# Optimization experiments

Measured on AMD Instinct MI355X. Metric: run time of the kernel, lower is better.

## Reference

```python
import jax, jax.numpy as jnp
import numpy as np

B = 8192; L = 50; D_EMB = 128
N_USER = 100000; N_MOVIE = 50000; N_DENSE = 8
D = 2 * D_EMB + D_EMB + N_DENSE  # 392 total_input_dim
E = 4; T = 2; H1 = 256; H2 = 128; ATT_H = 64; N_CROSS = 3


def setup_inputs() -> dict:
    key = jax.random.key(0)
    ks = jax.random.split(key, 28)
    rn = lambda k, shape, s=0.02: jax.random.normal(k, shape, jnp.float32) * s
    inp = {
        'userId': jax.random.randint(ks[0], (B,), 0, N_USER),
        'movieId': jax.random.randint(ks[1], (B,), 0, N_MOVIE),
        'seq_history': jax.random.randint(ks[2], (B, L), 0, N_MOVIE),
        'dense_feats': jax.random.normal(ks[3], (B, N_DENSE), jnp.float32),
        # embeddings (row 0 is padding_idx -> zeros)
        'emb_user': rn(ks[4], (N_USER + 1, D_EMB)).at[0].set(0.0),
        'emb_movie': rn(ks[5], (N_MOVIE + 1, D_EMB)).at[0].set(0.0),
        # DIN attention MLP: input [q,k,q-k,q*k] = 4*D_EMB
        'att_w1': rn(ks[6], (4 * D_EMB, ATT_H)), 'att_b1': jnp.zeros((ATT_H,), jnp.float32),
        'att_w2': rn(ks[7], (ATT_H, 1)), 'att_b2': jnp.zeros((1,), jnp.float32),
        # LayerNorms
        'in_gamma': jnp.ones((D,), jnp.float32), 'in_beta': jnp.zeros((D,), jnp.float32),
        'cr_gamma': jnp.ones((D,), jnp.float32), 'cr_beta': jnp.zeros((D,), jnp.float32),
        # CrossNetV2: x_{l+1} = x0 * (x_l W_l + b_l) + x_l
        'cross_W': rn(ks[8], (N_CROSS, D, D)), 'cross_b': jnp.zeros((N_CROSS, D), jnp.float32),
        # MMoE experts: Linear(D,H1)-ReLU-Linear(H1,H2), batched over E
        'exp_w1': rn(ks[9], (E, D, H1)), 'exp_b1': jnp.zeros((E, H1), jnp.float32),
        'exp_w2': rn(ks[10], (E, H1, H2)), 'exp_b2': jnp.zeros((E, H2), jnp.float32),
        # gates per task
        'gate_w': rn(ks[11], (T, D, E)), 'gate_b': jnp.zeros((T, E), jnp.float32),
        # task heads Linear(H2, 1)
        'head_w': rn(ks[12], (T, H2)), 'head_b': jnp.zeros((T,), jnp.float32),
    }
    return inp


def _layernorm(x, g, b, eps=1e-5):
    m = jnp.mean(x, axis=-1, keepdims=True)
    v = jnp.var(x, axis=-1, keepdims=True)
    return (x - m) * jax.lax.rsqrt(v + eps) * g + b


def _forward(userId, movieId, seq_history, dense_feats, emb_user, emb_movie,
             att_w1, att_b1, att_w2, att_b2, in_gamma, in_beta,
             cross_W, cross_b, cr_gamma, cr_beta,
             exp_w1, exp_b1, exp_w2, exp_b2, gate_w, gate_b, head_w, head_b):
    # sparse embedding gathers
    user_e = emb_user[userId]            # [B, D_EMB]
    movie_e = emb_movie[movieId]         # [B, D_EMB]  (target item)
    hist = emb_movie[seq_history]        # [B, L, D_EMB]
    mask = seq_history > 0               # [B, L]

    # DIN attention pooling
    q = jnp.broadcast_to(movie_e[:, None, :], hist.shape)            # [B, L, D_EMB]
    att_in = jnp.concatenate([q, hist, q - hist, q * hist], axis=-1)  # [B, L, 4*D_EMB]
    scores = (jax.nn.relu(att_in @ att_w1 + att_b1) @ att_w2 + att_b2)[..., 0]  # [B, L]
    scores = jnp.where(mask, scores, -1e9)
    probs = jax.nn.softmax(scores, axis=-1)                           # [B, L]
    interest = jnp.einsum('bl,bld->bd', probs, hist)                  # [B, D_EMB]

    x = jnp.concatenate([user_e, movie_e, interest, dense_feats], axis=-1)  # [B, D]
    x = _layernorm(x, in_gamma, in_beta)

    # CrossNetV2
    x0 = x
    for l in range(N_CROSS):
        x = x0 * (x @ cross_W[l] + cross_b[l]) + x
    x = _layernorm(x, cr_gamma, cr_beta)

    # MMoE: batched expert GEMMs + per-task soft gates
    h = jax.nn.relu(jnp.einsum('bd,edh->ebh', x, exp_w1) + exp_b1[:, None, :])  # [E,B,H1]
    eo = jnp.einsum('ebh,eho->ebo', h, exp_w2) + exp_b2[:, None, :]             # [E,B,H2]
    g = jax.nn.softmax(jnp.einsum('bd,tde->tbe', x, gate_w) + gate_b[:, None, :], axis=-1)  # [T,B,E]
    task_feat = jnp.einsum('tbe,ebo->tbo', g, eo)                                # [T,B,H2]

    logits = jnp.einsum('tbo,to->tb', task_feat, head_w) + head_b[:, None]       # [T,B]
    return logits


def reference(userId, movieId, seq_history, dense_feats, emb_user, emb_movie,
              att_w1, att_b1, att_w2, att_b2, in_gamma, in_beta,
              cross_W, cross_b, cr_gamma, cr_beta,
              exp_w1, exp_b1, exp_w2, exp_b2, gate_w, gate_b, head_w, head_b):
    return _forward(userId, movieId, seq_history, dense_feats, emb_user, emb_movie,
                    att_w1, att_b1, att_w2, att_b2, in_gamma, in_beta,
                    cross_W, cross_b, cr_gamma, cr_beta,
                    exp_w1, exp_b1, exp_w2, exp_b2, gate_w, gate_b, head_w, head_b)
```

## Files before the change

kernel.cpp:

```cpp
#include <hip/hip_runtime.h>
#include <hip/hip_bf16.h>

typedef short short8 __attribute__((ext_vector_type(8)));
typedef short short4v __attribute__((ext_vector_type(4)));
typedef float f32x4 __attribute__((ext_vector_type(4)));

constexpr int BB = 8192;
constexpr int LL = 50;
constexpr int DE = 128;
constexpr int DD = 392;
constexpr int HH1 = 256;
constexpr int HH2 = 128;

__device__ __forceinline__ short f2b(float x) {
    __hip_bfloat16 h = __float2bfloat16(x);
    return __builtin_bit_cast(short, h);
}
__device__ __forceinline__ float b2f(short v) {
    unsigned u = ((unsigned)(unsigned short)v) << 16;
    return __builtin_bit_cast(float, u);
}

constexpr int S0 = 3 * 392 * 392;
constexpr int S1 = 4 * 392 * 256;
constexpr int S2 = (50001 * 128) / 4;
constexpr int NB_TRANS = 9619;
constexpr int QC0 = 36 + NB_TRANS;
constexpr int NB_PREP = QC0 + 2048;

__global__ __launch_bounds__(256) void prep_all(
    const float* __restrict__ w1,
    const float* __restrict__ w2, const float* __restrict__ b2,
    const float* __restrict__ head_w, const float* __restrict__ att_b1,
    const float* __restrict__ cross_W, const float* __restrict__ exp_w1,
    const float* __restrict__ emb_movie, const int* __restrict__ movieId,
    float* __restrict__ WkpFf, float* __restrict__ hw2, float* __restrict__ hc,
    short* __restrict__ WTc, short* __restrict__ WT1, short* __restrict__ embB,
    float* __restrict__ qcAll)
{
    __shared__ float sh[4][128];
    const int blk = blockIdx.x, t = threadIdx.x;

    if (blk < 32) {
        int o = blk * 256 + t;
        int e = o & 7, lane = (o >> 3) & 63, nt = (o >> 9) & 3, kt = o >> 11;
        int k = (kt << 5) + ((lane >> 4) << 3) + e;
        int h = (nt << 4) + (lane & 15);
        int base = (o >> 3) << 4;
        WkpFf[base + e]     = w1[(128 + k) * 64 + h] - w1[(256 + k) * 64 + h];
        WkpFf[base + 8 + e] = w1[(384 + k) * 64 + h];
    } else if (blk < 36) {
        const int e = blk - 32;
        float* hw = &sh[0][0];
        hw[t] = head_w[t];
        __syncthreads();
        const float* row = &w2[((long)e * HH1 + t) * HH2];
        float s0 = 0.f, s1 = 0.f;
        #pragma unroll 8
        for (int o = 0; o < 128; o += 4) {
            float4 v = *reinterpret_cast<const float4*>(&row[o]);
            s0 += v.x * hw[o] + v.y * hw[o + 1] + v.z * hw[o + 2] + v.w * hw[o + 3];
            s1 += v.x * hw[128 + o] + v.y * hw[129 + o] + v.z * hw[130 + o] + v.w * hw[131 + o];
        }
        hw2[(((e << 8) + t) << 1) + 0] = s0;
        hw2[(((e << 8) + t) << 1) + 1] = s1;
        if (t < 2) {
            float s = 0.f;
            for (int o = 0; o < 128; ++o) s += b2[e * 128 + o] * hw[t * 128 + o];
            hc[e * 2 + t] = s;
        }
    } else if (blk < QC0) {
        int idx = (blk - 36) * 256 + t;
        if (idx < S0) {
            int z = idx / (392 * 392), rr = idx - z * 392 * 392;
            int c = rr / 392, r = rr - c * 392;
            WTc[idx] = f2b(cross_W[(long)z * 153664 + r * 392 + c]);
        } else if (idx < S0 + S1) {
            int j = idx - S0;
            int z = j / 100352, rr = j - z * 100352;
            int c = rr / 392, r = rr - c * 392;
            WT1[j] = f2b(exp_w1[(long)z * 100352 + r * 256 + c]);
        } else if (idx < S0 + S1 + S2) {
            long j = (long)(idx - S0 - S1) << 2;
            float4 v = *reinterpret_cast<const float4*>(&emb_movie[j]);
            short4v o;
            o[0] = f2b(v.x); o[1] = f2b(v.y); o[2] = f2b(v.z); o[3] = f2b(v.w);
            *reinterpret_cast<short4v*>(&embB[j]) = o;
        }
    } else {
        const int w = t >> 6, lane = t & 63;
        const int b = (blk - QC0) * 4 + w;
        if (lane < 32)
            *reinterpret_cast<float4*>(&sh[w][lane << 2]) =
                *reinterpret_cast<const float4*>(
                    &emb_movie[(long)movieId[b] * DE + (lane << 2)]);
        __syncthreads();
        float s = att_b1[lane];
        #pragma unroll 8
        for (int d = 0; d < 128; ++d)
            s = fmaf(sh[w][d], w1[d * 64 + lane] + w1[16384 + d * 64 + lane], s);
        qcAll[((long)b << 6) + lane] = s;
    }
}

__global__ __launch_bounds__(256, 8) void attn_kernel(
    const int* __restrict__ userId, const int* __restrict__ movieId,
    const int* __restrict__ seq, const float* __restrict__ dense,
    const float* __restrict__ emb_user, const float* __restrict__ emb_movie,
    const short* __restrict__ embB,
    const float* __restrict__ qcAll, const float* __restrict__ WkpFf,
    const float* __restrict__ att_w2, const float* __restrict__ att_b2,
    const float* __restrict__ in_gamma, const float* __restrict__ in_beta,
    float* __restrict__ x0f, short* __restrict__ x0b)
{
    __shared__ short hist[64 * 128];
    __shared__ float qs[128];
    __shared__ int   seq_s[64];
    __shared__ float spS[4][64];
    __shared__ float probs[64];
    __shared__ float ibuf[4][128];
    __shared__ float stats[2];

    const int b = blockIdx.x;
    const int t = threadIdx.x;
    const int lane = t & 63;
    const int w = t >> 6;

    if (t < 128) qs[t] = emb_movie[(long)movieId[b] * DE + t];
    if (t < 64)  seq_s[t] = (t < LL) ? seq[b * LL + t] : 0;
    __syncthreads();

    #pragma unroll
    for (int i = 0; i < 4; ++i) {
        const int idx = t + (i << 8);
        const int l = idx >> 4, c = idx & 15;
        short8 hv = *reinterpret_cast<const short8*>(&embB[(long)seq_s[l] * DE + (c << 3)]);
        const int byte = (l << 8) + ((c << 4) ^ ((l & 7) << 4));
        *reinterpret_cast<short8*>(reinterpret_cast<char*>(hist) + byte) = hv;
    }

    const int col = (w << 4) + (lane & 15);
    float ue = (t < 128) ? emb_user[(long)userId[b] * DE + t] : 0.f;
    float dv = (t >= 128 && t < 136) ? dense[b * 8 + (t - 128)] : 0.f;
    const float qc  = qcAll[((long)b << 6) + col];
    const float w2v = att_w2[col];

    short8 bfrag[4];
    #pragma unroll
    for (int kt = 0; kt < 4; ++kt) {
        const float* wkp = &WkpFf[((((kt << 2) + w) << 6) | lane) << 4];
        const int kq = (kt << 5) + ((lane >> 4) << 3);
        #pragma unroll
        for (int j = 0; j < 8; ++j)
            bfrag[kt][j] = f2b(fmaf(qs[kq + j], wkp[8 + j], wkp[j]));
    }
    __syncthreads();

    #pragma unroll
    for (int mt = 0; mt < 4; ++mt) {
        f32x4 acc = {0.f, 0.f, 0.f, 0.f};
        const int row = (mt << 4) + (lane & 15);
        const int rbase = row << 8;
        const int swz = (row & 7) << 4;
        #pragma unroll
        for (int kt = 0; kt < 4; ++kt) {
            const int kbyte = (kt << 6) + ((lane >> 4) << 4);
            short8 a = *reinterpret_cast<const short8*>(
                reinterpret_cast<char*>(hist) + rbase + (kbyte ^ swz));
            acc = __builtin_amdgcn_mfma_f32_16x16x32_bf16(a, bfrag[kt], acc, 0, 0, 0);
        }
        #pragma unroll
        for (int r = 0; r < 4; ++r) {
            float v = fmaxf(acc[r] + qc, 0.f) * w2v;
            v += __shfl_xor(v, 1); v += __shfl_xor(v, 2);
            v += __shfl_xor(v, 4); v += __shfl_xor(v, 8);
            if ((lane & 15) == 0)
                spS[w][(mt << 4) + ((lane >> 4) << 2) + r] = v;
        }
    }
    __syncthreads();

    if (t < 64) {
        float sc = spS[0][t] + spS[1][t] + spS[2][t] + spS[3][t] + att_b2[0];
        float s = (t < LL) ? ((seq_s[t] > 0) ? sc : -1e9f) : -INFINITY;
        float m = s;
        #pragma unroll
        for (int off = 32; off > 0; off >>= 1) m = fmaxf(m, __shfl_xor(m, off));
        float e = (t < LL) ? __expf(s - m) : 0.f;
        float sum = e;
        #pragma unroll
        for (int off = 32; off > 0; off >>= 1) sum += __shfl_xor(sum, off);
        probs[t] = (t < LL) ? (e / sum) : 0.f;
    }
    __syncthreads();

    const int g  = t >> 5;
    const int d0 = (t & 31) << 2;
    float4 ps = make_float4(0.f, 0.f, 0.f, 0.f);
    #pragma unroll
    for (int i = 0; i < 8; ++i) {
        const int l = g + (i << 3);
        const int byte = (l << 8) + ((d0 << 1) ^ ((l & 7) << 4));
        short4v hv = *reinterpret_cast<const short4v*>(
            reinterpret_cast<const char*>(hist) + byte);
        const float p = probs[l];
        ps.x = fmaf(p, b2f(hv[0]), ps.x);
        ps.y = fmaf(p, b2f(hv[1]), ps.y);
        ps.z = fmaf(p, b2f(hv[2]), ps.z);
        ps.w = fmaf(p, b2f(hv[3]), ps.w);
    }
    ps.x += __shfl_xor(ps.x, 32); ps.y += __shfl_xor(ps.y, 32);
    ps.z += __shfl_xor(ps.z, 32); ps.w += __shfl_xor(ps.w, 32);
    if (lane < 32)
        *reinterpret_cast<float4*>(&ibuf[w][(lane & 31) << 2]) = ps;
    __syncthreads();

    float v0 = (t < 128) ? ue : qs[t - 128];
    float v1 = 0.f;
    if (t < 128)       v1 = ibuf[0][t] + ibuf[1][t] + ibuf[2][t] + ibuf[3][t];
    else if (t < 136)  v1 = dv;

    float s2 = v0 + v1, q2 = v0 * v0 + v1 * v1;
    #pragma unroll
    for (int off = 32; off > 0; off >>= 1) {
        s2 += __shfl_xor(s2, off);
        q2 += __shfl_xor(q2, off);
    }
    if (lane == 0) { spS[0][w] = s2; spS[1][w] = q2; }
    __syncthreads();
    if (t == 0) {
        float S = spS[0][0] + spS[0][1] + spS[0][2] + spS[0][3];
        float Q = spS[1][0] + spS[1][1] + spS[1][2] + spS[1][3];
        float mean = S / (float)DD;
        float var = Q / (float)DD - mean * mean;
        stats[0] = mean;
        stats[1] = rsqrtf(var + 1e-5f);
    }
    __syncthreads();
    const float mean = stats[0], inv = stats[1];
    const long base = (long)b * DD;
    float o0 = (v0 - mean) * inv * in_gamma[t] + in_beta[t];
    x0f[base + t] = o0; x0b[base + t] = f2b(o0);
    if (t < 136) {
        float o1 = (v1 - mean) * inv * in_gamma[256 + t] + in_beta[256 + t];
        x0f[base + 256 + t] = o1; x0b[base + 256 + t] = f2b(o1);
    }
}

template<int MODE, int WF32, int WB16, int NXB, int NZB>
__global__ __launch_bounds__(256) void bgemm(
    const short* __restrict__ A, const short* __restrict__ WT,
    const float* __restrict__ bias,
    float* __restrict__ outF, short* __restrict__ outB,
    const float* __restrict__ x0, const float* __restrict__ xin,
    int M, int N, int K, long aZ, long wZ, long bZ, long oZ)
{
    __shared__ short As[2][64 * 64];
    __shared__ short Bs[2][64 * 64];

    int id = blockIdx.x;
    const int qq = (int)gridDim.x >> 3;
    id = (id & 7) * qq + (id >> 3);
    const int mb  = id / (NXB * NZB);
    const int rem = id - mb * (NXB * NZB);
    const int z   = rem / NXB;
    const int xb  = rem - z * NXB;

    A += (long)z * aZ; WT += (long)z * wZ; bias += (long)z * bZ;
    const long oz = (long)z * oZ;

    const int t = threadIdx.x, w = t >> 6, lane = t & 63;
    const int m0 = mb * 64, n0 = xb * 64;
    const int sm = t >> 3, sk8 = (t & 7) << 3;

    f32x4 acc[4];
    #pragma unroll
    for (int i = 0; i < 4; ++i) {
        #pragma unroll
        for (int r = 0; r < 4; ++r) acc[i][r] = 0.f;
    }

    const int nsteps = (K + 63) >> 6;
    short8 avA[2], bvA[2];

    auto loadA = [&](int k0) {
        #pragma unroll
        for (int i = 0; i < 2; ++i) {
            const int r = sm + (i << 5);
            short8 zv = {0, 0, 0, 0, 0, 0, 0, 0};
            avA[i] = zv; bvA[i] = zv;
            if (k0 + sk8 < K) {
                avA[i] = *reinterpret_cast<const short8*>(&A[(long)(m0 + r) * K + k0 + sk8]);
                if (n0 + r < N)
                    bvA[i] = *reinterpret_cast<const short8*>(&WT[(long)(n0 + r) * K + k0 + sk8]);
            }
        }
    };
    auto wrA = [&](int buf) {
        #pragma unroll
        for (int i = 0; i < 2; ++i) {
            const int r = sm + (i << 5);
            const int byte = (r << 7) + ((sk8 << 1) ^ ((r & 7) << 4));
            *reinterpret_cast<short8*>(reinterpret_cast<char*>(&As[buf][0]) + byte) = avA[i];
            *reinterpret_cast<short8*>(reinterpret_cast<char*>(&Bs[buf][0]) + byte) = bvA[i];
        }
    };
    auto domfma = [&](int buf) {
        #pragma unroll
        for (int kt = 0; kt < 2; ++kt) {
            const int kbyte = (kt << 6) + ((lane >> 4) << 4);
            const int ar = (w << 4) + (lane & 15);
            short8 a = *reinterpret_cast<const short8*>(
                reinterpret_cast<char*>(&As[buf][0]) + (ar << 7) + (kbyte ^ ((ar & 7) << 4)));
            #pragma unroll
            for (int nt = 0; nt < 4; ++nt) {
                const int br = (nt << 4) + (lane & 15);
                short8 bb = *reinterpret_cast<const short8*>(
                    reinterpret_cast<char*>(&Bs[buf][0]) + (br << 7) + (kbyte ^ ((br & 7) << 4)));
                acc[nt] = __builtin_amdgcn_mfma_f32_16x16x32_bf16(a, bb, acc[nt], 0, 0, 0);
            }
        }
    };

    loadA(0);
    wrA(0);
    if (nsteps > 1) loadA(64);
    __syncthreads();

    int cur = 0;
    for (int s = 0; s + 1 < nsteps; ++s) {
        domfma(cur);
        wrA(cur ^ 1);
        if (s + 2 < nsteps) loadA((s + 2) << 6);
        __syncthreads();
        cur ^= 1;
    }
    domfma(cur);

    #pragma unroll
    for (int nt = 0; nt < 4; ++nt) {
        const int col = n0 + (nt << 4) + (lane & 15);
        if (col < N) {
            const float bv = bias[col];
            #pragma unroll
            for (int r = 0; r < 4; ++r) {
                const int row = m0 + (w << 4) + ((lane >> 4) << 2) + r;
                float v = acc[nt][r] + bv;
                if (MODE == 1) v = fmaxf(v, 0.f);
                const long o = (long)row * N + col;
                if (MODE == 2) v = x0[o] * v + xin[o];
                if (WF32) outF[oz + o] = v;
                if (WB16) outB[oz + o] = f2b(v);
            }
        }
    }
}

__global__ __launch_bounds__(256) void ln_kernel(
    const float* __restrict__ in,
    const float* __restrict__ gamma, const float* __restrict__ beta,
    short* __restrict__ outB)
{
    __shared__ float red[2][4];
    __shared__ float stats[2];
    const int b = blockIdx.x, t = threadIdx.x, lane = t & 63, w = t >> 6;
    const long base = (long)b * DD;
    float v0 = in[base + t];
    float v1 = (t < 136) ? in[base + 256 + t] : 0.f;
    float s = v0 + v1, q2 = v0 * v0 + v1 * v1;
    #pragma unroll
    for (int off = 32; off > 0; off >>= 1) {
        s += __shfl_xor(s, off);
        q2 += __shfl_xor(q2, off);
    }
    if (lane == 0) { red[0][w] = s; red[1][w] = q2; }
    __syncthreads();
    if (t == 0) {
        float S = red[0][0] + red[0][1] + red[0][2] + red[0][3];
        float Q = red[1][0] + red[1][1] + red[1][2] + red[1][3];
        float mean = S / (float)DD;
        float var = Q / (float)DD - mean * mean;
        stats[0] = mean;
        stats[1] = rsqrtf(var + 1e-5f);
    }
    __syncthreads();
    const float mean = stats[0], inv = stats[1];
    outB[base + t] = f2b((v0 - mean) * inv * gamma[t] + beta[t]);
    if (t < 136)
        outB[base + 256 + t] = f2b((v1 - mean) * inv * gamma[256 + t] + beta[256 + t]);
}

__global__ __launch_bounds__(256) void final_kernel(
    const short* __restrict__ x, const short* __restrict__ h1,
    const float* __restrict__ hw2, const float* __restrict__ hc,
    const float* __restrict__ gate_w, const float* __restrict__ gate_b,
    const float* __restrict__ head_b, float* __restrict__ out)
{
    const int t = threadIdx.x, lane = t & 63, w = t >> 6;
    const int b = blockIdx.x * 4 + w;
    const short* xr = x + (long)b * DD;

    float xv[7];
    #pragma unroll
    for (int i = 0; i < 7; ++i) {
        int d = lane + (i << 6);
        xv[i] = (d < DD) ? b2f(xr[d]) : 0.f;
    }

    float gl[8] = {0.f, 0.f, 0.f, 0.f, 0.f, 0.f, 0.f, 0.f};
    #pragma unroll
    for (int i = 0; i < 7; ++i) {
        int d = lane + (i << 6);
        if (d < DD) {
            float4 g0 = *reinterpret_cast<const float4*>(&gate_w[d << 2]);
            float4 g1 = *reinterpret_cast<const float4*>(&gate_w[1568 + (d << 2)]);
            gl[0] = fmaf(xv[i], g0.x, gl[0]); gl[1] = fmaf(xv[i], g0.y, gl[1]);
            gl[2] = fmaf(xv[i], g0.z, gl[2]); gl[3] = fmaf(xv[i], g0.w, gl[3]);
            gl[4] = fmaf(xv[i], g1.x, gl[4]); gl[5] = fmaf(xv[i], g1.y, gl[5]);
            gl[6] = fmaf(xv[i], g1.z, gl[6]); gl[7] = fmaf(xv[i], g1.w, gl[7]);
        }
    }

    float ed[8];
    #pragma unroll
    for (int e = 0; e < 4; ++e) {
        short4v hv = *reinterpret_cast<const short4v*>(
            &h1[((long)e * BB + b) * HH1 + (lane << 2)]);
        const float* hwp = &hw2[(((e << 8) + (lane << 2))) << 1];
        float4 w01 = *reinterpret_cast<const float4*>(hwp);
        float4 w23 = *reinterpret_cast<const float4*>(hwp + 4);
        float h0 = b2f(hv[0]), h1f = b2f(hv[1]), h2 = b2f(hv[2]), h3 = b2f(hv[3]);
        ed[e]     = fmaf(h0, w01.x, fmaf(h1f, w01.z, fmaf(h2, w23.x, h3 * w23.z)));
        ed[4 + e] = fmaf(h0, w01.y, fmaf(h1f, w01.w, fmaf(h2, w23.y, h3 * w23.w)));
    }

    #pragma unroll
    for (int v = 0; v < 8; ++v) {
        #pragma unroll
        for (int off = 32; off > 0; off >>= 1) {
            gl[v] += __shfl_xor(gl[v], off);
            ed[v] += __shfl_xor(ed[v], off);
        }
    }

    if (lane == 0) {
        float res[2];
        #pragma unroll
        for (int tt = 0; tt < 2; ++tt) {
            float lv[4], m = -1e30f;
            #pragma unroll
            for (int e = 0; e < 4; ++e) {
                lv[e] = gl[tt * 4 + e] + gate_b[tt * 4 + e];
                m = fmaxf(m, lv[e]);
            }
            float sum = 0.f, acc = 0.f;
            #pragma unroll
            for (int e = 0; e < 4; ++e) { lv[e] = __expf(lv[e] - m); sum += lv[e]; }
            #pragma unroll
            for (int e = 0; e < 4; ++e)
                acc = fmaf(lv[e], ed[tt * 4 + e] + hc[e * 2 + tt], acc);
            res[tt] = head_b[tt] + acc / sum;
        }
        out[b] = res[0];
        out[BB + b] = res[1];
    }
}

extern "C" void kernel_launch(void* const* d_in, const int* in_sizes, int n_in,
                              void* d_out, int out_size, void* d_ws, size_t ws_size,
                              hipStream_t stream) {
    const int*   userId    = (const int*)d_in[0];
    const int*   movieId   = (const int*)d_in[1];
    const int*   seq       = (const int*)d_in[2];
    const float* dense     = (const float*)d_in[3];
    const float* emb_user  = (const float*)d_in[4];
    const float* emb_movie = (const float*)d_in[5];
    const float* att_w1    = (const float*)d_in[6];
    const float* att_b1    = (const float*)d_in[7];
    const float* att_w2    = (const float*)d_in[8];
    const float* att_b2    = (const float*)d_in[9];
    const float* in_gamma  = (const float*)d_in[10];
    const float* in_beta   = (const float*)d_in[11];
    const float* cr_gamma  = (const float*)d_in[12];
    const float* cr_beta   = (const float*)d_in[13];
    const float* cross_W   = (const float*)d_in[14];
    const float* cross_b   = (const float*)d_in[15];
    const float* exp_w1    = (const float*)d_in[16];
    const float* exp_b1    = (const float*)d_in[17];
    const float* exp_w2    = (const float*)d_in[18];
    const float* exp_b2    = (const float*)d_in[19];
    const float* gate_w    = (const float*)d_in[20];
    const float* gate_b    = (const float*)d_in[21];
    const float* head_w    = (const float*)d_in[22];
    const float* head_b    = (const float*)d_in[23];
    float* outp = (float*)d_out;

    char* p = (char*)d_ws;
    auto alloc = [&](size_t bytes) -> char* {
        char* r = p; p += (bytes + 255) & ~(size_t)255; return r;
    };
    float* WkpFf = (float*)alloc(16384 * 4);
    float* hw2 = (float*)alloc(2048 * 4);
    float* hc  = (float*)alloc(8 * 4);
    short* WTc = (short*)alloc((size_t)3 * 392 * 392 * 2);
    short* WT1 = (short*)alloc((size_t)4 * 256 * 392 * 2);
    short* embB = (short*)alloc((size_t)50001 * 128 * 2);
    float* qcAll = (float*)alloc((size_t)BB * 64 * 4);
    float* x0f = (float*)alloc((size_t)BB * DD * 4);
    short* x0b = (short*)alloc((size_t)BB * DD * 2);
    float* xAf = (float*)alloc((size_t)BB * DD * 4);
    short* xAb = (short*)alloc((size_t)BB * DD * 2);
    float* xBf = (float*)alloc((size_t)BB * DD * 4);
    short* xBb = (short*)alloc((size_t)BB * DD * 2);
    float* xCf = (float*)alloc((size_t)BB * DD * 4);
    short* xDb = (short*)alloc((size_t)BB * DD * 2);
    short* h1b = (short*)alloc((size_t)4 * BB * HH1 * 2);

    prep_all<<<NB_PREP, 256, 0, stream>>>(
        att_w1, exp_w2, exp_b2, head_w, att_b1, cross_W, exp_w1,
        emb_movie, movieId, WkpFf, hw2, hc, WTc, WT1, embB, qcAll);

    attn_kernel<<<BB, 256, 0, stream>>>(userId, movieId, seq, dense,
                                        emb_user, emb_movie, embB,
                                        qcAll, WkpFf, att_w2, att_b2,
                                        in_gamma, in_beta, x0f, x0b);

    bgemm<2, 1, 1, 7, 1><<<896, 256, 0, stream>>>(x0b, WTc, cross_b, xAf, xAb,
                                                  x0f, x0f, BB, DD, DD, 0, 0, 0, 0);
    bgemm<2, 1, 1, 7, 1><<<896, 256, 0, stream>>>(xAb, WTc + 392 * 392, cross_b + 392,
                                                  xBf, xBb, x0f, xAf, BB, DD, DD, 0, 0, 0, 0);
    bgemm<2, 1, 0, 7, 1><<<896, 256, 0, stream>>>(xBb, WTc + 2 * 392 * 392, cross_b + 784,
                                                  xCf, nullptr, x0f, xBf, BB, DD, DD, 0, 0, 0, 0);

    ln_kernel<<<BB, 256, 0, stream>>>(xCf, cr_gamma, cr_beta, xDb);

    bgemm<1, 0, 1, 4, 4><<<2048, 256, 0, stream>>>(
        xDb, WT1, exp_b1, nullptr, h1b, nullptr, nullptr,
        BB, HH1, DD, 0, (long)HH1 * DD, HH1, (long)BB * HH1);

    final_kernel<<<BB / 4, 256, 0, stream>>>(xDb, h1b, hw2, hc,
                                             gate_w, gate_b, head_b, outp);

    (void)in_sizes; (void)n_in; (void)out_size; (void)ws_size;
}
```

Measured before the change: 177.3 us.

## Enlarge GEMM block tile to 256x64 with 4x4 MFMA register tiling

The batched GEMM now computes a 256x64 output tile per block, with each wave owning a 64x64 sub-tile held in 16 accumulators, and the K step drops to 32. The LDS layout changes to a k-slice-major arrangement with no swizzle. The aim is more reuse of each B fragment across M tiles and less redundant global traffic per FLOP. The cost is higher register pressure and a quarter as many blocks (224 per cross layer), which may leave many CUs idle on a large-CU GPU, plus possible LDS bank conflicts now that the XOR swizzle is gone.

```diff
diff --git a/kernel.cpp b/kernel.cpp
--- a/kernel.cpp
+++ b/kernel.cpp
@@ -248,15 +248,15 @@
 }
 
 template<int MODE, int WF32, int WB16, int NXB, int NZB>
-__global__ __launch_bounds__(256) void bgemm(
+__global__ __launch_bounds__(256) void bgemm2(
     const short* __restrict__ A, const short* __restrict__ WT,
     const float* __restrict__ bias,
     float* __restrict__ outF, short* __restrict__ outB,
     const float* __restrict__ x0, const float* __restrict__ xin,
     int M, int N, int K, long aZ, long wZ, long bZ, long oZ)
 {
-    __shared__ short As[2][64 * 64];
-    __shared__ short Bs[2][64 * 64];
+    __shared__ short As[2][4][256][8];
+    __shared__ short Bs[2][4][64][8];
 
     int id = blockIdx.x;
     const int qq = (int)gridDim.x >> 3;
@@ -270,68 +270,71 @@
     const long oz = (long)z * oZ;
 
     const int t = threadIdx.x, w = t >> 6, lane = t & 63;
-    const int m0 = mb * 64, n0 = xb * 64;
-    const int sm = t >> 3, sk8 = (t & 7) << 3;
-
-    f32x4 acc[4];
-    #pragma unroll
-    for (int i = 0; i < 4; ++i) {
-        #pragma unroll
-        for (int r = 0; r < 4; ++r) acc[i][r] = 0.f;
-    }
-
-    const int nsteps = (K + 63) >> 6;
-    short8 avA[2], bvA[2];
-
-    auto loadA = [&](int k0) {
-        #pragma unroll
-        for (int i = 0; i < 2; ++i) {
-            const int r = sm + (i << 5);
+    const int m0 = mb * 256, n0 = xb * 64;
+    const int brow = t >> 2, bks = t & 3;
+
+    f32x4 acc[4][4];
+    #pragma unroll
+    for (int i = 0; i < 4; ++i)
+        #pragma unroll
+        for (int j = 0; j < 4; ++j)
+            #pragma unroll
+            for (int r = 0; r < 4; ++r) acc[i][j][r] = 0.f;
+
+    const int nsteps = (K + 31) >> 5;
+    short8 avr[4], bvr;
+
+    auto loadr = [&](int k0) {
+        #pragma unroll
+        for (int i = 0; i < 4; ++i) {
+            const int c = t + (i << 8);
+            const int row = c >> 2, ks = c & 3;
+            const int kk = k0 + (ks << 3);
             short8 zv = {0, 0, 0, 0, 0, 0, 0, 0};
-            avA[i] = zv; bvA[i] = zv;
-            if (k0 + sk8 < K) {
-                avA[i] = *reinterpret_cast<const short8*>(&A[(long)(m0 + r) * K + k0 + sk8]);
-                if (n0 + r < N)
-                    bvA[i] = *reinterpret_cast<const short8*>(&WT[(long)(n0 + r) * K + k0 + sk8]);
-            }
-        }
+            avr[i] = (kk < K)
+                ? *reinterpret_cast<const short8*>(&A[(long)(m0 + row) * K + kk]) : zv;
+        }
+        const int kkb = k0 + (bks << 3);
+        short8 zv = {0, 0, 0, 0, 0, 0, 0, 0};
+        bvr = (kkb < K && n0 + brow < N)
+            ? *reinterpret_cast<const short8*>(&WT[(long)(n0 + brow) * K + kkb]) : zv;
     };
-    auto wrA = [&](int buf) {
-        #pragma unroll
-        for (int i = 0; i < 2; ++i) {
-            const int r = sm + (i << 5);
-            const int byte = (r << 7) + ((sk8 << 1) ^ ((r & 7) << 4));
-            *reinterpret_cast<short8*>(reinterpret_cast<char*>(&As[buf][0]) + byte) = avA[i];
-            *reinterpret_cast<short8*>(reinterpret_cast<char*>(&Bs[buf][0]) + byte) = bvA[i];
-        }
+    auto wr = [&](int buf) {
+        #pragma unroll
+        for (int i = 0; i < 4; ++i) {
+            const int c = t + (i << 8);
+            const int row = c >> 2, ks = c & 3;
+            *reinterpret_cast<short8*>(&As[buf][ks][row][0]) = avr[i];
+        }
+        *reinterpret_cast<short8*>(&Bs[buf][bks][brow][0]) = bvr;
     };
     auto domfma = [&](int buf) {
-        #pragma unroll
-        for (int kt = 0; kt < 2; ++kt) {
-            const int kbyte = (kt << 6) + ((lane >> 4) << 4);
-            const int ar = (w << 4) + (lane & 15);
-            short8 a = *reinterpret_cast<const short8*>(
-                reinterpret_cast<char*>(&As[buf][0]) + (ar << 7) + (kbyte ^ ((ar & 7) << 4)));
+        const int ks = lane >> 4, l15 = lane & 15;
+        short8 bf[4];
+        #pragma unroll
+        for (int nt = 0; nt < 4; ++nt)
+            bf[nt] = *reinterpret_cast<const short8*>(&Bs[buf][ks][(nt << 4) + l15][0]);
+        #pragma unroll
+        for (int mt = 0; mt < 4; ++mt) {
+            short8 af = *reinterpret_cast<const short8*>(
+                &As[buf][ks][(w << 6) + (mt << 4) + l15][0]);
             #pragma unroll
-            for (int nt = 0; nt < 4; ++nt) {
-                const int br = (nt << 4) + (lane & 15);
-                short8 bb = *reinterpret_cast<const short8*>(
-                    reinterpret_cast<char*>(&Bs[buf][0]) + (br << 7) + (kbyte ^ ((br & 7) << 4)));
-                acc[nt] = __builtin_amdgcn_mfma_f32_16x16x32_bf16(a, bb, acc[nt], 0, 0, 0);
-            }
+            for (int nt = 0; nt < 4; ++nt)
+                acc[mt][nt] = __builtin_amdgcn_mfma_f32_16x16x32_bf16(
+                    af, bf[nt], acc[mt][nt], 0, 0, 0);
         }
     };
 
-    loadA(0);
-    wrA(0);
-    if (nsteps > 1) loadA(64);
+    loadr(0);
+    wr(0);
+    if (nsteps > 1) loadr(32);
     __syncthreads();
 
     int cur = 0;
     for (int s = 0; s + 1 < nsteps; ++s) {
         domfma(cur);
-        wrA(cur ^ 1);
-        if (s + 2 < nsteps) loadA((s + 2) << 6);
+        wr(cur ^ 1);
+        if (s + 2 < nsteps) loadr((s + 2) << 5);
         __syncthreads();
         cur ^= 1;
     }
@@ -339,18 +342,21 @@
 
     #pragma unroll
     for (int nt = 0; nt < 4; ++nt) {
-        const int col = n0 + (nt << 4) + (lane & 15);
-        if (col < N) {
-            const float bv = bias[col];
+        const int c = n0 + (nt << 4) + (lane & 15);
+        if (c < N) {
+            const float bv = bias[c];
             #pragma unroll
-            for (int r = 0; r < 4; ++r) {
-                const int row = m0 + (w << 4) + ((lane >> 4) << 2) + r;
-                float v = acc[nt][r] + bv;
-                if (MODE == 1) v = fmaxf(v, 0.f);
-                const long o = (long)row * N + col;
-                if (MODE == 2) v = x0[o] * v + xin[o];
-                if (WF32) outF[oz + o] = v;
-                if (WB16) outB[oz + o] = f2b(v);
+            for (int mt = 0; mt < 4; ++mt) {
+                #pragma unroll
+                for (int r = 0; r < 4; ++r) {
+                    const int row = m0 + (w << 6) + (mt << 4) + ((lane >> 4) << 2) + r;
+                    float v = acc[mt][nt][r] + bv;
+                    if (MODE == 1) v = fmaxf(v, 0.f);
+                    const long o = (long)row * N + c;
+                    if (MODE == 2) v = x0[o] * v + xin[o];
+                    if (WF32) outF[oz + o] = v;
+                    if (WB16) outB[oz + o] = f2b(v);
+                }
             }
         }
     }
@@ -525,16 +531,16 @@
                                         qcAll, WkpFf, att_w2, att_b2,
                                         in_gamma, in_beta, x0f, x0b);
 
-    bgemm<2, 1, 1, 7, 1><<<896, 256, 0, stream>>>(x0b, WTc, cross_b, xAf, xAb,
-                                                  x0f, x0f, BB, DD, DD, 0, 0, 0, 0);
-    bgemm<2, 1, 1, 7, 1><<<896, 256, 0, stream>>>(xAb, WTc + 392 * 392, cross_b + 392,
-                                                  xBf, xBb, x0f, xAf, BB, DD, DD, 0, 0, 0, 0);
-    bgemm<2, 1, 0, 7, 1><<<896, 256, 0, stream>>>(xBb, WTc + 2 * 392 * 392, cross_b + 784,
-                                                  xCf, nullptr, x0f, xBf, BB, DD, DD, 0, 0, 0, 0);
+    bgemm2<2, 1, 1, 7, 1><<<224, 256, 0, stream>>>(x0b, WTc, cross_b, xAf, xAb,
+                                                   x0f, x0f, BB, DD, DD, 0, 0, 0, 0);
+    bgemm2<2, 1, 1, 7, 1><<<224, 256, 0, stream>>>(xAb, WTc + 392 * 392, cross_b + 392,
+                                                   xBf, xBb, x0f, xAf, BB, DD, DD, 0, 0, 0, 0);
+    bgemm2<2, 1, 0, 7, 1><<<224, 256, 0, stream>>>(xBb, WTc + 2 * 392 * 392, cross_b + 784,
+                                                   xCf, nullptr, x0f, xBf, BB, DD, DD, 0, 0, 0, 0);
 
     ln_kernel<<<BB, 256, 0, stream>>>(xCf, cr_gamma, cr_beta, xDb);
 
-    bgemm<1, 0, 1, 4, 4><<<2048, 256, 0, stream>>>(
+    bgemm2<1, 0, 1, 4, 4><<<512, 256, 0, stream>>>(
         xDb, WT1, exp_b1, nullptr, h1b, nullptr, nullptr,
         BB, HH1, DD, 0, (long)HH1 * DD, HH1, (long)BB * HH1);
 
```

New measurement: 190.6 us. 1.08x slower.

## Fuse expert second layer and head projection into expert GEMM epilogue

Applied to the files above, without the earlier changes.

Adds a MODE 3 epilogue to the expert-layer GEMM. It applies ReLU, multiplies the activations by the precombined expert-head weights, and reduces them across lanes, writing per-column-block partial sums instead of the bf16 hidden activations. The final kernel then sums four partials per expert and task instead of reading the full 4×B×256 hidden tensor. This removes a large intermediate write and reread, at the cost of extra shuffles in the GEMM epilogue and a small partials buffer. It also leaves some dead code in the final kernel.

```diff
diff --git a/kernel.cpp b/kernel.cpp
--- a/kernel.cpp
+++ b/kernel.cpp
@@ -337,20 +337,59 @@
     }
     domfma(cur);
 
-    #pragma unroll
-    for (int nt = 0; nt < 4; ++nt) {
-        const int col = n0 + (nt << 4) + (lane & 15);
-        if (col < N) {
-            const float bv = bias[col];
+    if (MODE == 3) {
+        const int l15 = lane & 15, g = lane >> 4;
+        float pe[4][2];
+        #pragma unroll
+        for (int r = 0; r < 4; ++r) { pe[r][0] = 0.f; pe[r][1] = 0.f; }
+        #pragma unroll
+        for (int nt = 0; nt < 4; ++nt) {
+            const int c = n0 + (nt << 4) + l15;
+            const float bv = bias[c];
+            const float hw0 = x0[(((z << 8) + c) << 1) + 0];
+            const float hw1 = x0[(((z << 8) + c) << 1) + 1];
             #pragma unroll
             for (int r = 0; r < 4; ++r) {
-                const int row = m0 + (w << 4) + ((lane >> 4) << 2) + r;
-                float v = acc[nt][r] + bv;
-                if (MODE == 1) v = fmaxf(v, 0.f);
-                const long o = (long)row * N + col;
-                if (MODE == 2) v = x0[o] * v + xin[o];
-                if (WF32) outF[oz + o] = v;
-                if (WB16) outB[oz + o] = f2b(v);
+                float v = fmaxf(acc[nt][r] + bv, 0.f);
+                pe[r][0] = fmaf(v, hw0, pe[r][0]);
+                pe[r][1] = fmaf(v, hw1, pe[r][1]);
+            }
+        }
+        #pragma unroll
+        for (int r = 0; r < 4; ++r) {
+            #pragma unroll
+            for (int tt = 0; tt < 2; ++tt) {
+                float v = pe[r][tt];
+                v += __shfl_xor(v, 1); v += __shfl_xor(v, 2);
+                v += __shfl_xor(v, 4); v += __shfl_xor(v, 8);
+                pe[r][tt] = v;
+            }
+        }
+        if (l15 == 0) {
+            #pragma unroll
+            for (int r = 0; r < 4; ++r) {
+                const int row = m0 + (w << 4) + (g << 2) + r;
+                const long o = (long)(((xb << 2) | z) * BB + row) << 1;
+                outF[o + 0] = pe[r][0];
+                outF[o + 1] = pe[r][1];
+            }
+        }
+    } else {
+        #pragma unroll
+        for (int nt = 0; nt < 4; ++nt) {
+            const int c = n0 + (nt << 4) + (lane & 15);
+            if (c < N) {
+                const float bv = bias[c];
+                #pragma unroll
+                for (int r = 0; r < 4; ++r) {
+                    const int row = m0 + (w << 4) + ((lane >> 4) << 2) + r;
+                    float v = acc[nt][r] + bv;
+                    if (MODE == 1) v = fmaxf(v, 0.f);
+                    const long o = (long)row * N + c;
+                    if (MODE == 2) v = x0[o] * v + xin[o];
+                    if (WF32) outF[oz + o] = v;
+                    if (WB16) outB[oz + o] = f2b(v);
+                }
             }
         }
     }
@@ -391,8 +430,8 @@
 }
 
 __global__ __launch_bounds__(256) void final_kernel(
-    const short* __restrict__ x, const short* __restrict__ h1,
-    const float* __restrict__ hw2, const float* __restrict__ hc,
+    const short* __restrict__ x, const float* __restrict__ edPart,
+    const float* __restrict__ hc,
     const float* __restrict__ gate_w, const float* __restrict__ gate_b,
     const float* __restrict__ head_b, float* __restrict__ out)
 {
@@ -421,27 +460,31 @@
         }
     }
 
-    float ed[8];
-    #pragma unroll
-    for (int e = 0; e < 4; ++e) {
-        short4v hv = *reinterpret_cast<const short4v*>(
-            &h1[((long)e * BB + b) * HH1 + (lane << 2)]);
-        const float* hwp = &hw2[(((e << 8) + (lane << 2))) << 1];
-        float4 w01 = *reinterpret_cast<const float4*>(hwp);
-        float4 w23 = *reinterpret_cast<const float4*>(hwp + 4);
-        float h0 = b2f(hv[0]), h1f = b2f(hv[1]), h2 = b2f(hv[2]), h3 = b2f(hv[3]);
-        ed[e]     = fmaf(h0, w01.x, fmaf(h1f, w01.z, fmaf(h2, w23.x, h3 * w23.z)));
-        ed[4 + e] = fmaf(h0, w01.y, fmaf(h1f, w01.w, fmaf(h2, w23.y, h3 * w23.w)));
-    }
-
     #pragma unroll
     for (int v = 0; v < 8; ++v) {
         #pragma unroll
-        for (int off = 32; off > 0; off >>= 1) {
-            gl[v] += __shfl_xor(gl[v], off);
-            ed[v] += __shfl_xor(ed[v], off);
-        }
-    }
+        for (int off = 32; off > 0; off >>= 1) gl[v] += __shfl_xor(gl[v], off);
+    }
+
+    float edv = 0.f;
+    if (lane < 8) {
+        const int tt = lane >> 2, e = lane & 3;
+        #pragma unroll
+        for (int nb = 0; nb < 4; ++nb)
+            edv += edPart[((long)(((nb << 2) | e)) * BB + b) * 2 + tt];
+    }
+
+    if (lane == 0) {
+        float ed[8];
+        #pragma unroll
+        for (int v = 0; v < 8; ++v) {
+            ed[v] = 0.f;
+        }
+        (void)ed;
+    }
+    float edArr[8];
+    #pragma unroll
+    for (int v = 0; v < 8; ++v) edArr[v] = __shfl(edv, v);
 
     if (lane == 0) {
         float res[2];
@@ -458,7 +501,7 @@
             for (int e = 0; e < 4; ++e) { lv[e] = __expf(lv[e] - m); sum += lv[e]; }
             #pragma unroll
             for (int e = 0; e < 4; ++e)
-                acc = fmaf(lv[e], ed[tt * 4 + e] + hc[e * 2 + tt], acc);
+                acc = fmaf(lv[e], edArr[tt * 4 + e] + hc[e * 2 + tt], acc);
             res[tt] = head_b[tt] + acc / sum;
         }
         out[b] = res[0];
@@ -514,7 +557,7 @@
     short* xBb = (short*)alloc((size_t)BB * DD * 2);
     float* xCf = (float*)alloc((size_t)BB * DD * 4);
     short* xDb = (short*)alloc((size_t)BB * DD * 2);
-    short* h1b = (short*)alloc((size_t)4 * BB * HH1 * 2);
+    float* edPart = (float*)alloc((size_t)16 * BB * 2 * 4);
 
     prep_all<<<NB_PREP, 256, 0, stream>>>(
         att_w1, exp_w2, exp_b2, head_w, att_b1, cross_W, exp_w1,
@@ -534,11 +577,11 @@
 
     ln_kernel<<<BB, 256, 0, stream>>>(xCf, cr_gamma, cr_beta, xDb);
 
-    bgemm<1, 0, 1, 4, 4><<<2048, 256, 0, stream>>>(
-        xDb, WT1, exp_b1, nullptr, h1b, nullptr, nullptr,
-        BB, HH1, DD, 0, (long)HH1 * DD, HH1, (long)BB * HH1);
-
-    final_kernel<<<BB / 4, 256, 0, stream>>>(xDb, h1b, hw2, hc,
+    bgemm<3, 0, 0, 4, 4><<<2048, 256, 0, stream>>>(
+        xDb, WT1, exp_b1, edPart, nullptr, hw2, nullptr,
+        BB, HH1, DD, 0, (long)HH1 * DD, HH1, 0);
+
+    final_kernel<<<BB / 4, 256, 0, stream>>>(xDb, edPart, hc,
                                              gate_w, gate_b, head_b, outp);
 
     (void)in_sizes; (void)n_in; (void)out_size; (void)ws_size;
```

New measurement: 173.2 us. 1.02x faster.
